# Performance work log

Measured on AMD Instinct MI355X. Metric: run time of the kernel, lower is better.

## Reference

```python
import jax, jax.numpy as jnp
import numpy as np

DIM = 512
HEADS = 4
MARGIN = 1.0


def _attn_pool(x, Wq, bq, Wk, bk, Wv, bv, Wo, bo):
    # SelfAttention(video_dim, m_dim=DIM, heads=HEADS) followed by mean over time
    B, T, _ = x.shape
    hd = DIM // HEADS
    q = (x @ Wq + bq).reshape(B, T, HEADS, hd)
    k = (x @ Wk + bk).reshape(B, T, HEADS, hd)
    v = (x @ Wv + bv).reshape(B, T, HEADS, hd)
    a = jax.nn.softmax(jnp.einsum('bthd,bshd->bhts', q, k) / jnp.sqrt(jnp.float32(hd)), axis=-1)
    out = jnp.einsum('bhts,bshd->bthd', a, v).reshape(B, T, DIM) @ Wo + bo
    return out.mean(axis=1)  # [B, DIM]


def _ranking(x1, x2, gmask, margin):
    # vectorized form of the per-row torch.roll loop:
    # s[i, b] = <x1[b], x2[(b - i) mod B]>
    B = x1.shape[0]
    idx = (jnp.arange(B)[None, :] - jnp.arange(B)[:, None]) % B  # [B, B]
    s = jnp.einsum('bc,ibc->ib', x1, x2[idx])                    # [B, B]
    mask = gmask[idx] & gmask[None, :]                           # [B, B]
    # max-margin ranking loss with per-column masked mean, then mean over valid cols
    loss = jnp.maximum(0.0, margin + s[1:] - s[0:1])             # [B-1, B]
    m = mask[1:]
    cnt = m.sum(axis=0)
    col_mean = jnp.where(cnt > 0, (loss * m).sum(axis=0) / jnp.maximum(cnt, 1), 0.0)
    valid = cnt > 0
    loss_val = jnp.sum(col_mean * valid) / jnp.maximum(valid.sum(), 1)
    # ranking accuracy: idx==0 iff the true (row 0) score is max among selected
    sel_sum = jnp.sum(jnp.where(mask, s, 0.0), axis=0)
    col_valid = (sel_sum != 0) & mask.any(axis=0)
    s_masked = jnp.where(mask, s, -jnp.inf)
    top_is_first = (s[0] >= s_masked.max(axis=0)).astype(jnp.float32)
    acc = jnp.sum(jnp.where(col_valid, top_is_first, 0.0)) / jnp.maximum(col_valid.sum(), 1)
    return loss_val, jax.lax.stop_gradient(acc)


def setup_inputs() -> dict:
    key = jax.random.key(0)
    ks = iter(jax.random.split(key, 64))

    def nrm(shape, s=0.02):
        return jax.random.normal(next(ks), shape, jnp.float32) * s

    inp = {
        'o': jax.random.normal(next(ks), (128, 1024, DIM), jnp.float32),
        'rgb': jax.random.normal(next(ks), (128, 64, 2048), jnp.float32),
        'audio': jax.random.normal(next(ks), (128, 64, 128), jnp.float32),
        'group_mask': jax.random.randint(next(ks), (128,), 0, 2).astype(bool),
    }
    for name, d in (('rgb', 2048), ('audio', 128)):
        inp[f'{name}_Wq'] = nrm((d, DIM)); inp[f'{name}_bq'] = jnp.zeros((DIM,), jnp.float32)
        inp[f'{name}_Wk'] = nrm((d, DIM)); inp[f'{name}_bk'] = jnp.zeros((DIM,), jnp.float32)
        inp[f'{name}_Wv'] = nrm((d, DIM)); inp[f'{name}_bv'] = jnp.zeros((DIM,), jnp.float32)
        inp[f'{name}_Wo'] = nrm((DIM, DIM)); inp[f'{name}_bo'] = jnp.zeros((DIM,), jnp.float32)
        inp[f'{name}_W2'] = nrm((DIM, DIM)); inp[f'{name}_b2'] = jnp.zeros((DIM,), jnp.float32)
    inp['expand_W'] = nrm((DIM, 2 * DIM))
    inp['expand_b'] = jnp.zeros((2 * DIM,), jnp.float32)
    return inp


def reference(o, rgb, audio, group_mask,
              rgb_Wq, rgb_bq, rgb_Wk, rgb_bk, rgb_Wv, rgb_bv, rgb_Wo, rgb_bo, rgb_W2, rgb_b2,
              audio_Wq, audio_bq, audio_Wk, audio_bk, audio_Wv, audio_bv, audio_Wo, audio_bo,
              audio_W2, audio_b2, expand_W, expand_b):
    # per-modality encoders (CollaborativeGating multiplies are discarded in the
    # original forward, so gating is a no-op on the output -> skipped)
    f_rgb = _attn_pool(rgb, rgb_Wq, rgb_bq, rgb_Wk, rgb_bk, rgb_Wv, rgb_bv, rgb_Wo, rgb_bo) @ rgb_W2 + rgb_b2
    f_aud = _attn_pool(audio, audio_Wq, audio_bq, audio_Wk, audio_bk, audio_Wv, audio_bv, audio_Wo, audio_bo) @ audio_W2 + audio_b2
    feat = jnp.concatenate([f_rgb, f_aud], axis=-1)  # [B, 2*DIM]
    oo = o.mean(axis=-2) @ expand_W + expand_b       # [B, 2*DIM]
    oo = oo / jnp.maximum(jnp.linalg.norm(oo, axis=-1, keepdims=True), 1e-12)
    l1, a1 = _ranking(oo, feat, group_mask, MARGIN)
    l2, a2 = _ranking(feat, oo, group_mask, MARGIN)
    loss = l1 + l2
    acc = (a1 + a2) / 2.0
    return loss, acc
```

## Files before the change

kernel.cpp:

```cpp
#include <hip/hip_runtime.h>
#include <hip/hip_bf16.h>
#include <math.h>


using bf16x8 = __attribute__((ext_vector_type(8))) __bf16;
using f32x4  = __attribute__((ext_vector_type(4))) float;

enum : size_t {
  B_PART = 0,
  B_OM   = B_PART + (size_t)128*16*2*512*4,
  B_OO   = B_OM   + (size_t)128*512*4,
  B_G    = B_OO   + (size_t)128*1024*4,
  B_PP   = B_G    + (size_t)128*128*4,
  B_FEAT = B_PP   + (size_t)2*128*512*4,
  B_QBF  = B_FEAT + (size_t)2*128*512*4,
  B_KBF  = B_QBF  + (size_t)2*8192*512*2,
  B_VBF  = B_KBF  + (size_t)2*8192*512*2,
  B_XR   = B_VBF  + (size_t)2*8192*512*2,
  B_XA   = B_XR   + (size_t)8192*2048*2,
  B_WT   = B_XA   + (size_t)8192*128*2,
  B_END  = B_WT   + (size_t)3*512*2048*2 + (size_t)3*512*128*2
};

__device__ __forceinline__ unsigned short f2bf(float f) {
  __hip_bfloat16 h = __float2bfloat16(f);
  return __builtin_bit_cast(unsigned short, h);
}
__device__ __forceinline__ unsigned pack2(float a, float b) {
  return (unsigned)f2bf(a) | ((unsigned)f2bf(b) << 16);
}

struct PrepArgs {
  const float* o; float* part;
  const float* xr; unsigned short* xrb;
  const float* xa; unsigned short* xab;
  const float* w[6];
  unsigned short* wt[6];
};

__device__ __forceinline__ void castT64(const float* __restrict__ W,
                                        unsigned short* __restrict__ Wt,
                                        int K, int n0, int k0, int tid) {
  __shared__ float t[64][65];
  int c = tid & 63, r4 = tid >> 6;
#pragma unroll
  for (int i = 0; i < 16; ++i) {
    int r = r4 * 16 + i;
    t[c][r] = W[(size_t)(k0 + r) * 512 + n0 + c];
  }
  __syncthreads();
  int nr = tid >> 3, kk = (tid & 7) * 8;
#pragma unroll
  for (int p = 0; p < 2; ++p) {
    int n = nr + p * 32;
    float4 x0 = *(const float4*)&t[n][kk];
    float4 x1 = *(const float4*)&t[n][kk + 4];
    uint4 pk;
    pk.x = pack2(x0.x, x0.y); pk.y = pack2(x0.z, x0.w);
    pk.z = pack2(x1.x, x1.y); pk.w = pack2(x1.z, x1.w);
    *(uint4*)&Wt[(size_t)(n0 + n) * K + k0 + kk] = pk;
  }
}

__device__ __forceinline__ void cast8(const float* __restrict__ x,
                                      unsigned short* __restrict__ y,
                                      int i, int stride, int total) {
  for (; i < total; i += stride) {
    float4 v0 = *(const float4*)(x + (size_t)i * 8);
    float4 v1 = *(const float4*)(x + (size_t)i * 8 + 4);
    uint4 pk;
    pk.x = pack2(v0.x, v0.y); pk.y = pack2(v0.z, v0.w);
    pk.z = pack2(v1.x, v1.y); pk.w = pack2(v1.z, v1.w);
    *(uint4*)(y + (size_t)i * 8) = pk;
  }
}

__global__ __launch_bounds__(256) void prep_k(PrepArgs a) {
  int bid = blockIdx.x, tid = threadIdx.x;
  if (bid < 2048) {
    int c = bid & 15, b = bid >> 4;
    const float* base = a.o + ((size_t)b * 1024 + (size_t)c * 64) * 512;
    int d4 = (tid & 127) << 2, half = tid >> 7;
    float4 s = {0.f, 0.f, 0.f, 0.f};
    for (int t = half; t < 64; t += 2) {
      float4 v = *(const float4*)(base + (size_t)t * 512 + d4);
      s.x += v.x; s.y += v.y; s.z += v.z; s.w += v.w;
    }
    *(float4*)(a.part + (((size_t)b * 16 + c) * 2 + half) * 512 + d4) = s;
  } else if (bid < 2816) {
    int t = bid - 2048; int w = t >> 8; t &= 255;
    castT64(a.w[w], a.wt[w], 2048, (t >> 5) * 64, (t & 31) * 64, tid);
  } else if (bid < 2864) {
    int t = bid - 2816; int w = t >> 4; t &= 15;
    castT64(a.w[3 + w], a.wt[3 + w], 128, (t >> 1) * 64, (t & 1) * 64, tid);
  } else if (bid < 3888) {
    cast8(a.xr, a.xrb, (bid - 2864) * 256 + tid, 262144, 2097152);
  } else {
    cast8(a.xa, a.xab, (bid - 3888) * 256 + tid, 16384, 131072);
  }
}

__global__ __launch_bounds__(512) void finalize_mean_k(const float* __restrict__ part,
                                                       float* __restrict__ om) {
  int b = blockIdx.x, d = threadIdx.x;
  float s = 0.f;
  for (int c = 0; c < 32; ++c) s += part[((size_t)b * 32 + c) * 512 + d];
  om[(size_t)b * 512 + d] = s * (1.f / 1024.f);
}

__global__ __launch_bounds__(256) void gemm_f32_k(
    const float* __restrict__ A, int lda,
    const float* __restrict__ W, int ldw,
    const float* __restrict__ bias,
    float* __restrict__ C, int ldc, int K) {
  __shared__ float As[16][65];
  __shared__ float Ws[16][64];
  int tid = threadIdx.x;
  int tx = tid & 15, ty = tid >> 4;
  int row0 = blockIdx.y * 64, col0 = blockIdx.x * 64;
  float acc[4][4] = {};
  int ar = tid >> 2, ac = (tid & 3) << 2;
  int wr = tid >> 4, wc = (tid & 15) << 2;
  for (int k0 = 0; k0 < K; k0 += 16) {
    float4 av = *(const float4*)(A + (size_t)(row0 + ar) * lda + k0 + ac);
    As[ac + 0][ar] = av.x; As[ac + 1][ar] = av.y;
    As[ac + 2][ar] = av.z; As[ac + 3][ar] = av.w;
    float4 wv = *(const float4*)(W + (size_t)(k0 + wr) * ldw + col0 + wc);
    *(float4*)&Ws[wr][wc] = wv;
    __syncthreads();
#pragma unroll
    for (int k = 0; k < 16; ++k) {
      float a0 = As[k][(ty << 2) + 0], a1 = As[k][(ty << 2) + 1];
      float a2 = As[k][(ty << 2) + 2], a3 = As[k][(ty << 2) + 3];
      float4 w = *(const float4*)&Ws[k][tx << 2];
      acc[0][0] += a0 * w.x; acc[0][1] += a0 * w.y; acc[0][2] += a0 * w.z; acc[0][3] += a0 * w.w;
      acc[1][0] += a1 * w.x; acc[1][1] += a1 * w.y; acc[1][2] += a1 * w.z; acc[1][3] += a1 * w.w;
      acc[2][0] += a2 * w.x; acc[2][1] += a2 * w.y; acc[2][2] += a2 * w.z; acc[2][3] += a2 * w.w;
      acc[3][0] += a3 * w.x; acc[3][1] += a3 * w.y; acc[3][2] += a3 * w.z; acc[3][3] += a3 * w.w;
    }
    __syncthreads();
  }
  float4 bv = *(const float4*)(bias + col0 + (tx << 2));
#pragma unroll
  for (int i = 0; i < 4; ++i) {
    float4 ov;
    ov.x = acc[i][0] + bv.x; ov.y = acc[i][1] + bv.y;
    ov.z = acc[i][2] + bv.z; ov.w = acc[i][3] + bv.w;
    *(float4*)(C + (size_t)(row0 + (ty << 2) + i) * ldc + col0 + (tx << 2)) = ov;
  }
}

struct QkvAll {
  const unsigned short* A[2];
  const unsigned short* Wt[6];
  const float* bias[6];
  unsigned short* out[6];
};

__device__ __forceinline__ void stage16(const void* g, void* l) {
  __builtin_amdgcn_global_load_lds((const __attribute__((address_space(1))) void*)g,
                                   (__attribute__((address_space(3))) void*)l, 16, 0, 0);
}

__global__ __launch_bounds__(256) void qkv_k(QkvAll args) {
  __shared__ __align__(16) char smem[16384];
  unsigned short* As = (unsigned short*)smem;
  unsigned short* Bs = (unsigned short*)(smem + 8192);

  int id = blockIdx.x;
  int mi = id >= 768 ? 1 : 0; id -= mi * 768;
  int by = id & 63, bx = (id >> 6) & 3, bz = id >> 8;
  int K = mi ? 128 : 2048;
  const unsigned short* A = args.A[mi];
  int wi = mi * 3 + bz;
  const unsigned short* Bt = args.Wt[wi];
  const float* bias = args.bias[wi];

  int tid = threadIdx.x;
  int l = tid & 63, w = tid >> 6;
  int row0 = by * 128, col0 = bx * 128;
  int wrow = (w & 1) * 64, wcol = (w >> 1) * 64;
  int kg = l >> 4, lr = l & 15;

  f32x4 acc[4][4] = {};

  for (int k0 = 0; k0 < K; k0 += 32) {
#pragma unroll
    for (int i = 0; i < 2; ++i) {
      int c = w * 128 + i * 64 + l;
      int r = c >> 2, s = (c & 3) * 8;
      stage16(A + (size_t)(row0 + r) * K + k0 + s, smem + (size_t)(w * 128 + i * 64) * 16);
      stage16(Bt + (size_t)(col0 + r) * K + k0 + s, smem + 8192 + (size_t)(w * 128 + i * 64) * 16);
    }
    __syncthreads();
    bf16x8 af[4], bfr[4];
#pragma unroll
    for (int m = 0; m < 4; ++m) {
      af[m]  = *(const bf16x8*)(As + (size_t)(wrow + m * 16 + lr) * 32 + kg * 8);
      bfr[m] = *(const bf16x8*)(Bs + (size_t)(wcol + m * 16 + lr) * 32 + kg * 8);
    }
#pragma unroll
    for (int m = 0; m < 4; ++m)
#pragma unroll
      for (int n = 0; n < 4; ++n)
        acc[m][n] = __builtin_amdgcn_mfma_f32_16x16x32_bf16(af[m], bfr[n], acc[m][n], 0, 0, 0);
    __syncthreads();
  }

  float bv[4];
#pragma unroll
  for (int n = 0; n < 4; ++n) bv[n] = bias[col0 + wcol + n * 16 + lr];
  float* cst = (float*)(smem) + w * 1024;
  unsigned short* C = args.out[wi];
  int rr = l >> 3, q = l & 7;
#pragma unroll
  for (int m = 0; m < 4; ++m) {
#pragma unroll
    for (int n = 0; n < 4; ++n) {
      int g0 = (n * 16 + lr) >> 3, o0 = lr & 7;
#pragma unroll
      for (int j = 0; j < 4; ++j) {
        int row = kg * 4 + j;
        cst[row * 64 + (((g0 ^ (row & 7)) << 3) | o0)] = acc[m][n][j] + bv[n];
      }
    }
#pragma unroll
    for (int p = 0; p < 2; ++p) {
      int row = rr + p * 8;
      int grp = q ^ (row & 7);
      float4 x0 = *(const float4*)&cst[row * 64 + grp * 8];
      float4 x1 = *(const float4*)&cst[row * 64 + grp * 8 + 4];
      uint4 pk;
      pk.x = pack2(x0.x, x0.y); pk.y = pack2(x0.z, x0.w);
      pk.z = pack2(x1.x, x1.y); pk.w = pack2(x1.z, x1.w);
      *(uint4*)&C[(size_t)(row0 + wrow + m * 16 + row) * 512 + col0 + wcol + q * 8] = pk;
    }
  }
}

__global__ __launch_bounds__(256) void attn_pool_k(
    const unsigned short* __restrict__ qbf,
    const unsigned short* __restrict__ kbf,
    const unsigned short* __restrict__ vbf,
    float* __restrict__ pooled) {
  __shared__ float wlds[4][64];
  int b = blockIdx.x, m = blockIdx.y;
  int tid = threadIdx.x;
  int w = tid >> 6, l = tid & 63, lr = l & 15, g = l >> 4;
  size_t base = ((size_t)m * 8192 + (size_t)b * 64) * 512 + w * 128;

  bf16x8 qf[4][4];
#pragma unroll
  for (int tb = 0; tb < 4; ++tb)
#pragma unroll
    for (int ks = 0; ks < 4; ++ks)
      qf[tb][ks] = *(const bf16x8*)(qbf + base + (size_t)(tb * 16 + lr) * 512 + ks * 32 + g * 8);

  f32x4 acc[4][4] = {};
#pragma unroll
  for (int sb = 0; sb < 4; ++sb) {
    bf16x8 kf[4];
#pragma unroll
    for (int ks = 0; ks < 4; ++ks)
      kf[ks] = *(const bf16x8*)(kbf + base + (size_t)(sb * 16 + lr) * 512 + ks * 32 + g * 8);
#pragma unroll
    for (int tb = 0; tb < 4; ++tb)
#pragma unroll
      for (int ks = 0; ks < 4; ++ks)
        acc[sb][tb] = __builtin_amdgcn_mfma_f32_16x16x32_bf16(kf[ks], qf[tb][ks], acc[sb][tb], 0, 0, 0);
  }

  const float scale = 0.08838834764831845f;
  float mx[4] = {-INFINITY, -INFINITY, -INFINITY, -INFINITY};
#pragma unroll
  for (int sb = 0; sb < 4; ++sb)
#pragma unroll
    for (int tb = 0; tb < 4; ++tb)
#pragma unroll
      for (int j = 0; j < 4; ++j) {
        acc[sb][tb][j] *= scale;
        mx[tb] = fmaxf(mx[tb], acc[sb][tb][j]);
      }
#pragma unroll
  for (int tb = 0; tb < 4; ++tb) {
    mx[tb] = fmaxf(mx[tb], __shfl_xor(mx[tb], 16));
    mx[tb] = fmaxf(mx[tb], __shfl_xor(mx[tb], 32));
  }
  float sm[4] = {0.f, 0.f, 0.f, 0.f};
#pragma unroll
  for (int sb = 0; sb < 4; ++sb)
#pragma unroll
    for (int tb = 0; tb < 4; ++tb)
#pragma unroll
      for (int j = 0; j < 4; ++j) {
        float e = expf(acc[sb][tb][j] - mx[tb]);
        acc[sb][tb][j] = e;
        sm[tb] += e;
      }
  float inv[4];
#pragma unroll
  for (int tb = 0; tb < 4; ++tb) {
    sm[tb] += __shfl_xor(sm[tb], 16);
    sm[tb] += __shfl_xor(sm[tb], 32);
    inv[tb] = 1.f / sm[tb];
  }
#pragma unroll
  for (int sb = 0; sb < 4; ++sb)
#pragma unroll
    for (int j = 0; j < 4; ++j) {
      float cs = acc[sb][0][j] * inv[0] + acc[sb][1][j] * inv[1]
               + acc[sb][2][j] * inv[2] + acc[sb][3][j] * inv[3];
      cs += __shfl_xor(cs, 1);
      cs += __shfl_xor(cs, 2);
      cs += __shfl_xor(cs, 4);
      cs += __shfl_xor(cs, 8);
      if (lr == 0) wlds[w][sb * 16 + g * 4 + j] = cs * (1.f / 64.f);
    }
  __syncthreads();

  int h = tid >> 6, c2 = (tid & 63) << 1;
  size_t vbase = ((size_t)m * 8192 + (size_t)b * 64) * 512 + h * 128 + c2;
  float s0 = 0.f, s1 = 0.f;
#pragma unroll 8
  for (int s = 0; s < 64; ++s) {
    unsigned u = *(const unsigned*)(vbf + vbase + (size_t)s * 512);
    float vlo = __builtin_bit_cast(float, u << 16);
    float vhi = __builtin_bit_cast(float, u & 0xffff0000u);
    float wv = wlds[h][s];
    s0 += wv * vlo; s1 += wv * vhi;
  }
  float2 o2 = {s0, s1};
  *(float2*)(pooled + ((size_t)m * 128 + b) * 512 + h * 128 + c2) = o2;
}

__global__ __launch_bounds__(256) void pofeat_k(
    const float* __restrict__ pp,
    const float* __restrict__ Wo0, const float* __restrict__ bo0,
    const float* __restrict__ W20, const float* __restrict__ b20,
    const float* __restrict__ Wo1, const float* __restrict__ bo1,
    const float* __restrict__ W21, const float* __restrict__ b21,
    float* __restrict__ feat) {
  __shared__ __align__(16) float Ws[16][512];
  __shared__ unsigned short po[8][512];
  __shared__ float As[8][16];
  int m = blockIdx.y, rb = blockIdx.x;
  const float* Wo = m ? Wo1 : Wo0;
  const float* bo = m ? bo1 : bo0;
  const float* W2 = m ? W21 : W20;
  const float* b2 = m ? b21 : b20;
  int row0 = m * 128 + rb * 8;
  int tid = threadIdx.x;
  int r = tid >> 5, tx = tid & 31;

  float acc[16];
#pragma unroll
  for (int j = 0; j < 16; ++j) acc[j] = 0.f;
  for (int k0 = 0; k0 < 512; k0 += 16) {
    __syncthreads();
#pragma unroll
    for (int i = 0; i < 8; ++i) {
      int idx = (i * 256 + tid) * 4;
      *(float4*)&Ws[idx >> 9][idx & 511] =
          *(const float4*)(Wo + (size_t)(k0 + (idx >> 9)) * 512 + (idx & 511));
    }
    if (tid < 128) As[tid >> 4][tid & 15] = pp[(size_t)(row0 + (tid >> 4)) * 512 + k0 + (tid & 15)];
    __syncthreads();
#pragma unroll
    for (int k = 0; k < 16; ++k) {
      float a = As[r][k];
#pragma unroll
      for (int j = 0; j < 16; ++j) acc[j] += a * Ws[k][tx + 32 * j];
    }
  }
#pragma unroll
  for (int j = 0; j < 16; ++j) po[r][tx + 32 * j] = f2bf(acc[j] + bo[tx + 32 * j]);

#pragma unroll
  for (int j = 0; j < 16; ++j) acc[j] = 0.f;
  for (int k0 = 0; k0 < 512; k0 += 16) {
    __syncthreads();
#pragma unroll
    for (int i = 0; i < 8; ++i) {
      int idx = (i * 256 + tid) * 4;
      *(float4*)&Ws[idx >> 9][idx & 511] =
          *(const float4*)(W2 + (size_t)(k0 + (idx >> 9)) * 512 + (idx & 511));
    }
    __syncthreads();
#pragma unroll
    for (int k = 0; k < 16; ++k) {
      float a = __builtin_bit_cast(float, (unsigned)po[r][k0 + k] << 16);
#pragma unroll
      for (int j = 0; j < 16; ++j) acc[j] += a * Ws[k][tx + 32 * j];
    }
  }
#pragma unroll
  for (int j = 0; j < 16; ++j)
    feat[(size_t)(row0 + r) * 512 + tx + 32 * j] = acc[j] + b2[tx + 32 * j];
}

__global__ __launch_bounds__(256) void ntg_k(const float* __restrict__ oo,
                                             const float* __restrict__ feat,
                                             float* __restrict__ G) {
  __shared__ float As[16][33], Bs[16][33];
  __shared__ float inv32[32];
  int tid = threadIdx.x;
  int row0 = blockIdx.y * 32, col0 = blockIdx.x * 32;
  int ar = tid >> 3, aq = tid & 7;
  int ty = tid >> 4, tx = tid & 15;
  float acc[2][2] = {};
  float ssq = 0.f;
  for (int k0 = 0; k0 < 1024; k0 += 16) {
    float2 av = *(const float2*)(oo + (size_t)(row0 + ar) * 1024 + k0 + aq * 2);
    As[aq * 2 + 0][ar] = av.x;
    As[aq * 2 + 1][ar] = av.y;
    ssq += av.x * av.x + av.y * av.y;
    int kk = k0 + aq * 2;
    float2 bv = *(const float2*)(feat + (size_t)((kk >> 9) * 128 + col0 + ar) * 512 + (kk & 511));
    Bs[aq * 2 + 0][ar] = bv.x;
    Bs[aq * 2 + 1][ar] = bv.y;
    __syncthreads();
#pragma unroll
    for (int k = 0; k < 16; ++k) {
      float a0 = As[k][ty * 2], a1 = As[k][ty * 2 + 1];
      float b0 = Bs[k][tx * 2], b1 = Bs[k][tx * 2 + 1];
      acc[0][0] += a0 * b0; acc[0][1] += a0 * b1;
      acc[1][0] += a1 * b0; acc[1][1] += a1 * b1;
    }
    __syncthreads();
  }
  ssq += __shfl_xor(ssq, 1);
  ssq += __shfl_xor(ssq, 2);
  ssq += __shfl_xor(ssq, 4);
  if (aq == 0) inv32[ar] = 1.f / fmaxf(sqrtf(ssq), 1e-12f);
  __syncthreads();
#pragma unroll
  for (int i = 0; i < 2; ++i)
#pragma unroll
    for (int j = 0; j < 2; ++j)
      G[(size_t)(row0 + ty * 2 + i) * 128 + col0 + tx * 2 + j] = acc[i][j] * inv32[ty * 2 + i];
}

__global__ __launch_bounds__(128) void final_k(const float* __restrict__ G,
                                               const int* __restrict__ gmask,
                                               float* __restrict__ out) {
  __shared__ float cm[2][128], vd[2][128], tp[2][128], cv[2][128];
  __shared__ int gm[128];
  int b = threadIdx.x;
  gm[b] = gmask[b];
  __syncthreads();
  for (int r = 0; r < 2; ++r) {
    bool gb = gm[b] != 0;
    float s0 = G[b * 128 + b];
    int cnt = 0;
    float lsum = 0.f, selsum = 0.f, smax = -INFINITY;
    bool anym = false;
    for (int i = 0; i < 128; ++i) {
      int j = (b - i + 128) & 127;
      bool mk = gb && (gm[j] != 0);
      float sv = (r == 0) ? G[b * 128 + j] : G[j * 128 + b];
      if (mk) {
        selsum += sv; anym = true;
        smax = fmaxf(smax, sv);
        if (i >= 1) { cnt++; lsum += fmaxf(0.f, 1.f + sv - s0); }
      }
    }
    cm[r][b] = (cnt > 0) ? (lsum / (float)cnt) : 0.f;
    vd[r][b] = (cnt > 0) ? 1.f : 0.f;
    bool colvalid = (selsum != 0.f) && anym;
    tp[r][b] = (colvalid && (s0 >= smax)) ? 1.f : 0.f;
    cv[r][b] = colvalid ? 1.f : 0.f;
  }
  __syncthreads();
  if (b == 0) {
    float loss = 0.f, acc = 0.f;
    for (int r = 0; r < 2; ++r) {
      float scm = 0, svd = 0, stp = 0, scv = 0;
      for (int i = 0; i < 128; ++i) { scm += cm[r][i]; svd += vd[r][i]; stp += tp[r][i]; scv += cv[r][i]; }
      loss += scm / fmaxf(svd, 1.f);
      acc += stp / fmaxf(scv, 1.f);
    }
    out[0] = loss;
    out[1] = acc * 0.5f;
  }
}

extern "C" void kernel_launch(void* const* d_in, const int* in_sizes, int n_in,
                              void* d_out, int out_size, void* d_ws, size_t ws_size,
                              hipStream_t stream) {
  const float* o     = (const float*)d_in[0];
  const float* rgb   = (const float*)d_in[1];
  const float* audio = (const float*)d_in[2];
  const int* gmask   = (const int*)d_in[3];
  const float* W[2][10];
  for (int m = 0; m < 2; ++m)
    for (int w = 0; w < 10; ++w) W[m][w] = (const float*)d_in[4 + m * 10 + w];
  const float* expand_W = (const float*)d_in[24];
  const float* expand_b = (const float*)d_in[25];

  char* ws = (char*)d_ws;
  float* part = (float*)(ws + B_PART);
  float* om   = (float*)(ws + B_OM);
  float* oo   = (float*)(ws + B_OO);
  float* G    = (float*)(ws + B_G);
  float* pp2  = (float*)(ws + B_PP);
  float* feat2= (float*)(ws + B_FEAT);
  unsigned short* qbf = (unsigned short*)(ws + B_QBF);
  unsigned short* kbf = (unsigned short*)(ws + B_KBF);
  unsigned short* vbf = (unsigned short*)(ws + B_VBF);
  unsigned short* xrb = (unsigned short*)(ws + B_XR);
  unsigned short* xab = (unsigned short*)(ws + B_XA);
  unsigned short* wt  = (unsigned short*)(ws + B_WT);
  unsigned short* wtp[6];
  wtp[0] = wt;
  wtp[1] = wtp[0] + (size_t)512 * 2048;
  wtp[2] = wtp[1] + (size_t)512 * 2048;
  wtp[3] = wtp[2] + (size_t)512 * 2048;
  wtp[4] = wtp[3] + (size_t)512 * 128;
  wtp[5] = wtp[4] + (size_t)512 * 128;

  PrepArgs pa;
  pa.o = o;      pa.part = part;
  pa.xr = rgb;   pa.xrb = xrb;
  pa.xa = audio; pa.xab = xab;
  pa.w[0] = W[0][0]; pa.w[1] = W[0][2]; pa.w[2] = W[0][4];
  pa.w[3] = W[1][0]; pa.w[4] = W[1][2]; pa.w[5] = W[1][4];
  for (int i = 0; i < 6; ++i) pa.wt[i] = wtp[i];
  prep_k<<<3952, 256, 0, stream>>>(pa);

  finalize_mean_k<<<128, 512, 0, stream>>>(part, om);
  gemm_f32_k<<<dim3(16, 2), 256, 0, stream>>>(om, 512, expand_W, 1024, expand_b, oo, 1024, 512);

  QkvAll qa;
  qa.A[0] = xrb; qa.A[1] = xab;
  for (int i = 0; i < 6; ++i) qa.Wt[i] = wtp[i];
  qa.bias[0] = W[0][1]; qa.bias[1] = W[0][3]; qa.bias[2] = W[0][5];
  qa.bias[3] = W[1][1]; qa.bias[4] = W[1][3]; qa.bias[5] = W[1][5];
  qa.out[0] = qbf;                       qa.out[1] = kbf;                       qa.out[2] = vbf;
  qa.out[3] = qbf + (size_t)8192 * 512;  qa.out[4] = kbf + (size_t)8192 * 512;  qa.out[5] = vbf + (size_t)8192 * 512;
  qkv_k<<<1536, 256, 0, stream>>>(qa);

  attn_pool_k<<<dim3(128, 2), 256, 0, stream>>>(qbf, kbf, vbf, pp2);

  pofeat_k<<<dim3(16, 2), 256, 0, stream>>>(pp2,
      W[0][6], W[0][7], W[0][8], W[0][9],
      W[1][6], W[1][7], W[1][8], W[1][9], feat2);

  ntg_k<<<dim3(4, 4), 256, 0, stream>>>(oo, feat2, G);
  final_k<<<1, 128, 0, stream>>>(G, gmask, (float*)d_out);
}
```

Baseline: 446.4 us.

## Interleave o-mean reduction with QKV GEMM and split pofeat into tiled GEMMs

Moves the bandwidth-bound partial mean over `o` out of the prep kernel and into the QKV MFMA kernel. Each group of 448 blocks holds 192 GEMM tiles and 256 reduction tiles, so memory-bound and compute-bound work can share the GPU at the same time. It also replaces the fused pofeat kernel, which ran only 32 blocks with an 8-row tile, with two launches of a 64x64 tiled fp32 GEMM. These are 32 blocks each and keep the intermediate in fp32 instead of bf16. The cost is an extra launch and a po buffer round trip through global memory.

```diff
diff --git a/kernel.cpp b/kernel.cpp
--- a/kernel.cpp
+++ b/kernel.cpp
@@ -12,7 +12,8 @@
   B_OO   = B_OM   + (size_t)128*512*4,
   B_G    = B_OO   + (size_t)128*1024*4,
   B_PP   = B_G    + (size_t)128*128*4,
-  B_FEAT = B_PP   + (size_t)2*128*512*4,
+  B_PO   = B_PP   + (size_t)2*128*512*4,
+  B_FEAT = B_PO   + (size_t)2*128*512*4,
   B_QBF  = B_FEAT + (size_t)2*128*512*4,
   B_KBF  = B_QBF  + (size_t)2*8192*512*2,
   B_VBF  = B_KBF  + (size_t)2*8192*512*2,
@@ -31,7 +32,6 @@
 }
 
 struct PrepArgs {
-  const float* o; float* part;
   const float* xr; unsigned short* xrb;
   const float* xa; unsigned short* xab;
   const float* w[6];
@@ -77,26 +77,124 @@
 
 __global__ __launch_bounds__(256) void prep_k(PrepArgs a) {
   int bid = blockIdx.x, tid = threadIdx.x;
-  if (bid < 2048) {
-    int c = bid & 15, b = bid >> 4;
-    const float* base = a.o + ((size_t)b * 1024 + (size_t)c * 64) * 512;
+  if (bid < 768) {
+    int w = bid >> 8, t = bid & 255;
+    castT64(a.w[w], a.wt[w], 2048, (t >> 5) * 64, (t & 31) * 64, tid);
+  } else if (bid < 816) {
+    int t = bid - 768; int w = t >> 4; t &= 15;
+    castT64(a.w[3 + w], a.wt[3 + w], 128, (t >> 1) * 64, (t & 1) * 64, tid);
+  } else if (bid < 1840) {
+    cast8(a.xr, a.xrb, (bid - 816) * 256 + tid, 262144, 2097152);
+  } else {
+    cast8(a.xa, a.xab, (bid - 1840) * 256 + tid, 16384, 131072);
+  }
+}
+
+struct QkvAll {
+  const unsigned short* A[2];
+  const unsigned short* Wt[6];
+  const float* bias[6];
+  unsigned short* out[6];
+  const float* o; float* part;
+};
+
+__device__ __forceinline__ void stage16(const void* g, void* l) {
+  __builtin_amdgcn_global_load_lds((const __attribute__((address_space(1))) void*)g,
+                                   (__attribute__((address_space(3))) void*)l, 16, 0, 0);
+}
+
+__global__ __launch_bounds__(256) void qkv_mean_k(QkvAll args) {
+  __shared__ __align__(16) char smem[16384];
+
+  int id = blockIdx.x;
+  int blk = id / 448, off = id % 448;
+
+  if (off >= 192) {
+    int mb = blk * 256 + (off - 192);
+    int c = mb & 15, b = mb >> 4;
+    const float* base = args.o + ((size_t)b * 1024 + (size_t)c * 64) * 512;
+    int tid = threadIdx.x;
     int d4 = (tid & 127) << 2, half = tid >> 7;
     float4 s = {0.f, 0.f, 0.f, 0.f};
     for (int t = half; t < 64; t += 2) {
       float4 v = *(const float4*)(base + (size_t)t * 512 + d4);
       s.x += v.x; s.y += v.y; s.z += v.z; s.w += v.w;
     }
-    *(float4*)(a.part + (((size_t)b * 16 + c) * 2 + half) * 512 + d4) = s;
-  } else if (bid < 2816) {
-    int t = bid - 2048; int w = t >> 8; t &= 255;
-    castT64(a.w[w], a.wt[w], 2048, (t >> 5) * 64, (t & 31) * 64, tid);
-  } else if (bid < 2864) {
-    int t = bid - 2816; int w = t >> 4; t &= 15;
-    castT64(a.w[3 + w], a.wt[3 + w], 128, (t >> 1) * 64, (t & 1) * 64, tid);
-  } else if (bid < 3888) {
-    cast8(a.xr, a.xrb, (bid - 2864) * 256 + tid, 262144, 2097152);
-  } else {
-    cast8(a.xa, a.xab, (bid - 3888) * 256 + tid, 16384, 131072);
+    *(float4*)(args.part + (((size_t)b * 16 + c) * 2 + half) * 512 + d4) = s;
+    return;
+  }
+
+  int qid = blk * 192 + off;
+  unsigned short* As = (unsigned short*)smem;
+  unsigned short* Bs = (unsigned short*)(smem + 8192);
+
+  int mi = qid >= 768 ? 1 : 0; qid -= mi * 768;
+  int by = qid & 63, bx = (qid >> 6) & 3, bz = qid >> 8;
+  int K = mi ? 128 : 2048;
+  const unsigned short* A = args.A[mi];
+  int wi = mi * 3 + bz;
+  const unsigned short* Bt = args.Wt[wi];
+  const float* bias = args.bias[wi];
+
+  int tid = threadIdx.x;
+  int l = tid & 63, w = tid >> 6;
+  int row0 = by * 128, col0 = bx * 128;
+  int wrow = (w & 1) * 64, wcol = (w >> 1) * 64;
+  int kg = l >> 4, lr = l & 15;
+
+  f32x4 acc[4][4] = {};
+
+  for (int k0 = 0; k0 < K; k0 += 32) {
+#pragma unroll
+    for (int i = 0; i < 2; ++i) {
+      int c = w * 128 + i * 64 + l;
+      int r = c >> 2, s = (c & 3) * 8;
+      stage16(A + (size_t)(row0 + r) * K + k0 + s, smem + (size_t)(w * 128 + i * 64) * 16);
+      stage16(Bt + (size_t)(col0 + r) * K + k0 + s, smem + 8192 + (size_t)(w * 128 + i * 64) * 16);
+    }
+    __syncthreads();
+    bf16x8 af[4], bfr[4];
+#pragma unroll
+    for (int m = 0; m < 4; ++m) {
+      af[m]  = *(const bf16x8*)(As + (size_t)(wrow + m * 16 + lr) * 32 + kg * 8);
+      bfr[m] = *(const bf16x8*)(Bs + (size_t)(wcol + m * 16 + lr) * 32 + kg * 8);
+    }
+#pragma unroll
+    for (int m = 0; m < 4; ++m)
+#pragma unroll
+      for (int n = 0; n < 4; ++n)
+        acc[m][n] = __builtin_amdgcn_mfma_f32_16x16x32_bf16(af[m], bfr[n], acc[m][n], 0, 0, 0);
+    __syncthreads();
+  }
+
+  float bv[4];
+#pragma unroll
+  for (int n = 0; n < 4; ++n) bv[n] = bias[col0 + wcol + n * 16 + lr];
+  float* cst = (float*)(smem) + w * 1024;
+  unsigned short* C = args.out[wi];
+  int rr = l >> 3, q = l & 7;
+#pragma unroll
+  for (int m = 0; m < 4; ++m) {
+#pragma unroll
+    for (int n = 0; n < 4; ++n) {
+      int g0 = (n * 16 + lr) >> 3, o0 = lr & 7;
+#pragma unroll
+      for (int j = 0; j < 4; ++j) {
+        int row = kg * 4 + j;
+        cst[row * 64 + (((g0 ^ (row & 7)) << 3) | o0)] = acc[m][n][j] + bv[n];
+      }
+    }
+#pragma unroll
+    for (int p = 0; p < 2; ++p) {
+      int row = rr + p * 8;
+      int grp = q ^ (row & 7);
+      float4 x0 = *(const float4*)&cst[row * 64 + grp * 8];
+      float4 x1 = *(const float4*)&cst[row * 64 + grp * 8 + 4];
+      uint4 pk;
+      pk.x = pack2(x0.x, x0.y); pk.y = pack2(x0.z, x0.w);
+      pk.z = pack2(x1.x, x1.y); pk.w = pack2(x1.z, x1.w);
+      *(uint4*)&C[(size_t)(row0 + wrow + m * 16 + row) * 512 + col0 + wcol + q * 8] = pk;
+    }
   }
 }
 
@@ -150,91 +248,47 @@
   }
 }
 
-struct QkvAll {
-  const unsigned short* A[2];
-  const unsigned short* Wt[6];
-  const float* bias[6];
-  unsigned short* out[6];
-};
-
-__device__ __forceinline__ void stage16(const void* g, void* l) {
-  __builtin_amdgcn_global_load_lds((const __attribute__((address_space(1))) void*)g,
-                                   (__attribute__((address_space(3))) void*)l, 16, 0, 0);
-}
-
-__global__ __launch_bounds__(256) void qkv_k(QkvAll args) {
-  __shared__ __align__(16) char smem[16384];
-  unsigned short* As = (unsigned short*)smem;
-  unsigned short* Bs = (unsigned short*)(smem + 8192);
-
-  int id = blockIdx.x;
-  int mi = id >= 768 ? 1 : 0; id -= mi * 768;
-  int by = id & 63, bx = (id >> 6) & 3, bz = id >> 8;
-  int K = mi ? 128 : 2048;
-  const unsigned short* A = args.A[mi];
-  int wi = mi * 3 + bz;
-  const unsigned short* Bt = args.Wt[wi];
-  const float* bias = args.bias[wi];
-
+__global__ __launch_bounds__(256) void gemm_f32_2w_k(
+    const float* __restrict__ A,
+    const float* __restrict__ W0, const float* __restrict__ W1,
+    const float* __restrict__ b0, const float* __restrict__ b1,
+    float* __restrict__ C) {
+  const float* W = (blockIdx.y >= 2) ? W1 : W0;
+  const float* bias = (blockIdx.y >= 2) ? b1 : b0;
+  __shared__ float As[16][65];
+  __shared__ float Ws[16][64];
   int tid = threadIdx.x;
-  int l = tid & 63, w = tid >> 6;
-  int row0 = by * 128, col0 = bx * 128;
-  int wrow = (w & 1) * 64, wcol = (w >> 1) * 64;
-  int kg = l >> 4, lr = l & 15;
-
-  f32x4 acc[4][4] = {};
-
-  for (int k0 = 0; k0 < K; k0 += 32) {
-#pragma unroll
-    for (int i = 0; i < 2; ++i) {
-      int c = w * 128 + i * 64 + l;
-      int r = c >> 2, s = (c & 3) * 8;
-      stage16(A + (size_t)(row0 + r) * K + k0 + s, smem + (size_t)(w * 128 + i * 64) * 16);
-      stage16(Bt + (size_t)(col0 + r) * K + k0 + s, smem + 8192 + (size_t)(w * 128 + i * 64) * 16);
-    }
-    __syncthreads();
-    bf16x8 af[4], bfr[4];
-#pragma unroll
-    for (int m = 0; m < 4; ++m) {
-      af[m]  = *(const bf16x8*)(As + (size_t)(wrow + m * 16 + lr) * 32 + kg * 8);
-      bfr[m] = *(const bf16x8*)(Bs + (size_t)(wcol + m * 16 + lr) * 32 + kg * 8);
-    }
-#pragma unroll
-    for (int m = 0; m < 4; ++m)
-#pragma unroll
-      for (int n = 0; n < 4; ++n)
-        acc[m][n] = __builtin_amdgcn_mfma_f32_16x16x32_bf16(af[m], bfr[n], acc[m][n], 0, 0, 0);
-    __syncthreads();
-  }
-
-  float bv[4];
-#pragma unroll
-  for (int n = 0; n < 4; ++n) bv[n] = bias[col0 + wcol + n * 16 + lr];
-  float* cst = (float*)(smem) + w * 1024;
-  unsigned short* C = args.out[wi];
-  int rr = l >> 3, q = l & 7;
-#pragma unroll
-  for (int m = 0; m < 4; ++m) {
-#pragma unroll
-    for (int n = 0; n < 4; ++n) {
-      int g0 = (n * 16 + lr) >> 3, o0 = lr & 7;
-#pragma unroll
-      for (int j = 0; j < 4; ++j) {
-        int row = kg * 4 + j;
-        cst[row * 64 + (((g0 ^ (row & 7)) << 3) | o0)] = acc[m][n][j] + bv[n];
-      }
-    }
-#pragma unroll
-    for (int p = 0; p < 2; ++p) {
-      int row = rr + p * 8;
-      int grp = q ^ (row & 7);
-      float4 x0 = *(const float4*)&cst[row * 64 + grp * 8];
-      float4 x1 = *(const float4*)&cst[row * 64 + grp * 8 + 4];
-      uint4 pk;
-      pk.x = pack2(x0.x, x0.y); pk.y = pack2(x0.z, x0.w);
-      pk.z = pack2(x1.x, x1.y); pk.w = pack2(x1.z, x1.w);
-      *(uint4*)&C[(size_t)(row0 + wrow + m * 16 + row) * 512 + col0 + wcol + q * 8] = pk;
-    }
+  int tx = tid & 15, ty = tid >> 4;
+  int row0 = blockIdx.y * 64, col0 = blockIdx.x * 64;
+  float acc[4][4] = {};
+  int ar = tid >> 2, ac = (tid & 3) << 2;
+  int wr = tid >> 4, wc = (tid & 15) << 2;
+  for (int k0 = 0; k0 < 512; k0 += 16) {
+    float4 av = *(const float4*)(A + (size_t)(row0 + ar) * 512 + k0 + ac);
+    As[ac + 0][ar] = av.x; As[ac + 1][ar] = av.y;
+    As[ac + 2][ar] = av.z; As[ac + 3][ar] = av.w;
+    float4 wv = *(const float4*)(W + (size_t)(k0 + wr) * 512 + col0 + wc);
+    *(float4*)&Ws[wr][wc] = wv;
+    __syncthreads();
+#pragma unroll
+    for (int k = 0; k < 16; ++k) {
+      float a0 = As[k][(ty << 2) + 0], a1 = As[k][(ty << 2) + 1];
+      float a2 = As[k][(ty << 2) + 2], a3 = As[k][(ty << 2) + 3];
+      float4 w = *(const float4*)&Ws[k][tx << 2];
+      acc[0][0] += a0 * w.x; acc[0][1] += a0 * w.y; acc[0][2] += a0 * w.z; acc[0][3] += a0 * w.w;
+      acc[1][0] += a1 * w.x; acc[1][1] += a1 * w.y; acc[1][2] += a1 * w.z; acc[1][3] += a1 * w.w;
+      acc[2][0] += a2 * w.x; acc[2][1] += a2 * w.y; acc[2][2] += a2 * w.z; acc[2][3] += a2 * w.w;
+      acc[3][0] += a3 * w.x; acc[3][1] += a3 * w.y; acc[3][2] += a3 * w.z; acc[3][3] += a3 * w.w;
+    }
+    __syncthreads();
+  }
+  float4 bv = *(const float4*)(bias + col0 + (tx << 2));
+#pragma unroll
+  for (int i = 0; i < 4; ++i) {
+    float4 ov;
+    ov.x = acc[i][0] + bv.x; ov.y = acc[i][1] + bv.y;
+    ov.z = acc[i][2] + bv.z; ov.w = acc[i][3] + bv.w;
+    *(float4*)(C + (size_t)(row0 + (ty << 2) + i) * 512 + col0 + (tx << 2)) = ov;
   }
 }
 
@@ -331,71 +385,6 @@
   }
   float2 o2 = {s0, s1};
   *(float2*)(pooled + ((size_t)m * 128 + b) * 512 + h * 128 + c2) = o2;
-}
-
-__global__ __launch_bounds__(256) void pofeat_k(
-    const float* __restrict__ pp,
-    const float* __restrict__ Wo0, const float* __restrict__ bo0,
-    const float* __restrict__ W20, const float* __restrict__ b20,
-    const float* __restrict__ Wo1, const float* __restrict__ bo1,
-    const float* __restrict__ W21, const float* __restrict__ b21,
-    float* __restrict__ feat) {
-  __shared__ __align__(16) float Ws[16][512];
-  __shared__ unsigned short po[8][512];
-  __shared__ float As[8][16];
-  int m = blockIdx.y, rb = blockIdx.x;
-  const float* Wo = m ? Wo1 : Wo0;
-  const float* bo = m ? bo1 : bo0;
-  const float* W2 = m ? W21 : W20;
-  const float* b2 = m ? b21 : b20;
-  int row0 = m * 128 + rb * 8;
-  int tid = threadIdx.x;
-  int r = tid >> 5, tx = tid & 31;
-
-  float acc[16];
-#pragma unroll
-  for (int j = 0; j < 16; ++j) acc[j] = 0.f;
-  for (int k0 = 0; k0 < 512; k0 += 16) {
-    __syncthreads();
-#pragma unroll
-    for (int i = 0; i < 8; ++i) {
-      int idx = (i * 256 + tid) * 4;
-      *(float4*)&Ws[idx >> 9][idx & 511] =
-          *(const float4*)(Wo + (size_t)(k0 + (idx >> 9)) * 512 + (idx & 511));
-    }
-    if (tid < 128) As[tid >> 4][tid & 15] = pp[(size_t)(row0 + (tid >> 4)) * 512 + k0 + (tid & 15)];
-    __syncthreads();
-#pragma unroll
-    for (int k = 0; k < 16; ++k) {
-      float a = As[r][k];
-#pragma unroll
-      for (int j = 0; j < 16; ++j) acc[j] += a * Ws[k][tx + 32 * j];
-    }
-  }
-#pragma unroll
-  for (int j = 0; j < 16; ++j) po[r][tx + 32 * j] = f2bf(acc[j] + bo[tx + 32 * j]);
-
-#pragma unroll
-  for (int j = 0; j < 16; ++j) acc[j] = 0.f;
-  for (int k0 = 0; k0 < 512; k0 += 16) {
-    __syncthreads();
-#pragma unroll
-    for (int i = 0; i < 8; ++i) {
-      int idx = (i * 256 + tid) * 4;
-      *(float4*)&Ws[idx >> 9][idx & 511] =
-          *(const float4*)(W2 + (size_t)(k0 + (idx >> 9)) * 512 + (idx & 511));
-    }
-    __syncthreads();
-#pragma unroll
-    for (int k = 0; k < 16; ++k) {
-      float a = __builtin_bit_cast(float, (unsigned)po[r][k0 + k] << 16);
-#pragma unroll
-      for (int j = 0; j < 16; ++j) acc[j] += a * Ws[k][tx + 32 * j];
-    }
-  }
-#pragma unroll
-  for (int j = 0; j < 16; ++j)
-    feat[(size_t)(row0 + r) * 512 + tx + 32 * j] = acc[j] + b2[tx + 32 * j];
 }
 
 __global__ __launch_bounds__(256) void ntg_k(const float* __restrict__ oo,
@@ -503,6 +492,7 @@
   float* oo   = (float*)(ws + B_OO);
   float* G    = (float*)(ws + B_G);
   float* pp2  = (float*)(ws + B_PP);
+  float* po2  = (float*)(ws + B_PO);
   float* feat2= (float*)(ws + B_FEAT);
   unsigned short* qbf = (unsigned short*)(ws + B_QBF);
   unsigned short* kbf = (unsigned short*)(ws + B_KBF);
@@ -519,16 +509,12 @@
   wtp[5] = wtp[4] + (size_t)512 * 128;
 
   PrepArgs pa;
-  pa.o = o;      pa.part = part;
   pa.xr = rgb;   pa.xrb = xrb;
   pa.xa = audio; pa.xab = xab;
   pa.w[0] = W[0][0]; pa.w[1] = W[0][2]; pa.w[2] = W[0][4];
   pa.w[3] = W[1][0]; pa.w[4] = W[1][2]; pa.w[5] = W[1][4];
   for (int i = 0; i < 6; ++i) pa.wt[i] = wtp[i];
-  prep_k<<<3952, 256, 0, stream>>>(pa);
-
-  finalize_mean_k<<<128, 512, 0, stream>>>(part, om);
-  gemm_f32_k<<<dim3(16, 2), 256, 0, stream>>>(om, 512, expand_W, 1024, expand_b, oo, 1024, 512);
+  prep_k<<<1904, 256, 0, stream>>>(pa);
 
   QkvAll qa;
   qa.A[0] = xrb; qa.A[1] = xab;
@@ -537,13 +523,16 @@
   qa.bias[3] = W[1][1]; qa.bias[4] = W[1][3]; qa.bias[5] = W[1][5];
   qa.out[0] = qbf;                       qa.out[1] = kbf;                       qa.out[2] = vbf;
   qa.out[3] = qbf + (size_t)8192 * 512;  qa.out[4] = kbf + (size_t)8192 * 512;  qa.out[5] = vbf + (size_t)8192 * 512;
-  qkv_k<<<1536, 256, 0, stream>>>(qa);
+  qa.o = o; qa.part = part;
+  qkv_mean_k<<<3584, 256, 0, stream>>>(qa);
+
+  finalize_mean_k<<<128, 512, 0, stream>>>(part, om);
+  gemm_f32_k<<<dim3(16, 2), 256, 0, stream>>>(om, 512, expand_W, 1024, expand_b, oo, 1024, 512);
 
   attn_pool_k<<<dim3(128, 2), 256, 0, stream>>>(qbf, kbf, vbf, pp2);
 
-  pofeat_k<<<dim3(16, 2), 256, 0, stream>>>(pp2,
-      W[0][6], W[0][7], W[0][8], W[0][9],
-      W[1][6], W[1][7], W[1][8], W[1][9], feat2);
+  gemm_f32_2w_k<<<dim3(8, 4), 256, 0, stream>>>(pp2, W[0][6], W[1][6], W[0][7], W[1][7], po2);
+  gemm_f32_2w_k<<<dim3(8, 4), 256, 0, stream>>>(po2, W[0][8], W[1][8], W[0][9], W[1][9], feat2);
 
   ntg_k<<<dim3(4, 4), 256, 0, stream>>>(oo, feat2, G);
   final_k<<<1, 128, 0, stream>>>(G, gmask, (float*)d_out);
```

Result: faster. 393.6 us (-11.8%).
